# Kernel optimization log

Hardware: AMD Instinct MI355X
Metric: run time of the kernel (lower is better)

The kernel has to match this reference:

```python
import jax, jax.numpy as jnp
import numpy as np

H = 512        # hidden_size
E = 512        # embedding_size
VOCAB = 32
OPS = 16
B = 64         # batch of trees
N = 1023       # complete binary tree, depth 9 (2^10 - 1 nodes)
TEMP = 3.0
INT_TYPES_MAX = 1  # types 0 (INT_PO) and 1 (INT_NE) carry a numeric arg


def setup_inputs() -> dict:
    key = jax.random.key(0)
    ks = jax.random.split(key, 12)
    s = 0.05
    return {
        "node_types": jax.random.randint(ks[0], (B, N), 0, VOCAB),
        "node_args": jax.random.normal(ks[1], (B, N), jnp.float32),
        "validity_mask": jax.random.uniform(ks[2], (B, OPS), jnp.float32, 1e-3, 1.0),
        "emb_table": jax.random.normal(ks[3], (VOCAB, E), jnp.float32) * s,
        "W_ih": jax.random.normal(ks[4], (8 * H, E), jnp.float32) * s,
        "W_hh": jax.random.normal(ks[5], (8 * H, 2 * H), jnp.float32) * s,
        "b_ih": jax.random.normal(ks[6], (8 * H,), jnp.float32) * s,
        "b_hh": jax.random.normal(ks[7], (8 * H,), jnp.float32) * s,
        "W1": jax.random.normal(ks[8], (H, H), jnp.float32) * s,
        "b1": jax.random.normal(ks[9], (H,), jnp.float32) * s,
        "W2": jax.random.normal(ks[10], (OPS, H), jnp.float32) * s,
        "b2": jax.random.normal(ks[11], (OPS,), jnp.float32) * s,
    }


def reference(node_types, node_args, validity_mask, emb_table,
              W_ih, W_hh, b_ih, b_hh, W1, b1, W2, b2):
    # --- SympleEmbedding: per-node embedding; int-typed nodes carry arg in last slot
    emb = emb_table[node_types]                                   # [B, N, E]
    is_int = node_types <= INT_TYPES_MAX                          # [B, N]
    emb = emb.at[..., -1].set(jnp.where(is_int, node_args, emb[..., -1]))

    # --- BinaryTreeLSTM, batched level-by-level (heap layout: children of i are 2i+1, 2i+2)
    D = int(np.log2(N + 1)) - 1                                   # depth of internal levels-1 = 9
    h = jnp.zeros((B, N, H), emb.dtype)                           # leaves: zeros
    c = jnp.zeros((B, N, H), emb.dtype)
    bias = b_ih + b_hh
    for d in range(D - 1, -1, -1):                                # bottom-up over internal levels
        idx = np.arange(2 ** d - 1, 2 ** (d + 1) - 1)             # nodes at level d
        left, right = 2 * idx + 1, 2 * idx + 2
        h0 = jnp.concatenate([h[:, left], h[:, right]], axis=-1)  # [B, n, 2H]
        c0 = jnp.concatenate([c[:, left], c[:, right]], axis=-1)
        gates = (jnp.einsum('bne,ge->bng', emb[:, idx], W_ih)
                 + jnp.einsum('bnh,gh->bng', h0, W_hh) + bias)    # [B, n, 8H]
        i_g, f_g, g_g, o_g = jnp.split(gates, 4, axis=-1)         # torch LSTM gate order i,f,g,o
        c_new = jax.nn.sigmoid(f_g) * c0 + jax.nn.sigmoid(i_g) * jnp.tanh(g_g)
        h_new = jax.nn.sigmoid(o_g) * jnp.tanh(c_new)
        h = h.at[:, idx].set(h_new[..., :H])                      # keep first H (as in module)
        c = c.at[:, idx].set(c_new[..., :H])

    # --- actor FFN on root hidden + validity-masked tempered softmax
    root_h = h[:, 0]                                              # [B, H]
    x = jax.nn.relu(root_h @ W1.T + b1)
    logits = x @ W2.T + b2 + jnp.log(validity_mask)
    return jax.nn.softmax(logits / TEMP, axis=-1)                 # [B, OPS]
```

## Files before the change

kernel.cpp:

```cpp
#include <hip/hip_runtime.h>
#include <hip/hip_cooperative_groups.h>
#include <math.h>

namespace cg = cooperative_groups;

#define Nn 1023

typedef __attribute__((ext_vector_type(8))) short short8;
typedef __attribute__((ext_vector_type(4))) float f32x4;

#define AS1(p) ((const __attribute__((address_space(1))) void*)(p))
#define AS3(p) ((__attribute__((address_space(3))) void*)(p))

__device__ __forceinline__ float sigf(float x) { return 1.0f / (1.0f + __expf(-x)); }
__device__ __forceinline__ float tanhfast(float x) {
    float e = __expf(2.0f * x);
    return 1.0f - 2.0f / (e + 1.0f);
}
__device__ __forceinline__ unsigned short f2bf(float x) {
    unsigned u = __float_as_uint(x);
    return (unsigned short)((u + 0x7fffu + ((u >> 16) & 1u)) >> 16);
}
__device__ __forceinline__ float bf2f(unsigned short b) {
    return __uint_as_float(((unsigned)b) << 16);
}

__global__ __launch_bounds__(256) void prep_all(
    const float* __restrict__ W_hh, unsigned short* __restrict__ WhT,
    const float* __restrict__ W1, float* __restrict__ W1t,
    const int* __restrict__ node_types, const float* __restrict__ node_args,
    const float* __restrict__ emb, const float* __restrict__ W2,
    float* __restrict__ W2t, int* __restrict__ tyv, float* __restrict__ alphaf,
    const float* __restrict__ W_ih, const float* __restrict__ b_ih,
    const float* __restrict__ b_hh, float* __restrict__ E32b,
    float* __restrict__ w511f, int* __restrict__ rowidx, int* __restrict__ cnt) {
    int bid = blockIdx.x, t = threadIdx.x;
    if (bid < 1024) {
        int idx = bid * 256 + t;
        int P = idx >> 7;
        int k0 = (idx & 127) * 8;
        int row = ((P >> 4) & 3) * 1024 + (P >> 6) * 16 + (P & 15);
        const float* src = W_hh + (size_t)row * 1024 + k0;
        float4 v0 = *(const float4*)src;
        float4 v1 = *(const float4*)(src + 4);
        short8 o;
        o[0] = (short)f2bf(v0.x); o[1] = (short)f2bf(v0.y);
        o[2] = (short)f2bf(v0.z); o[3] = (short)f2bf(v0.w);
        o[4] = (short)f2bf(v1.x); o[5] = (short)f2bf(v1.y);
        o[6] = (short)f2bf(v1.z); o[7] = (short)f2bf(v1.w);
        *(short8*)(WhT + (size_t)P * 1024 + k0) = o;
    } else if (bid < 1088) {
        __shared__ float tile[64][65];
        int idx2 = bid - 1024;
        int jb = (idx2 & 7) * 64, kb = (idx2 >> 3) * 64;
        #pragma unroll
        for (int i = 0; i < 16; ++i) {
            int idx = t + i * 256;
            int lj = idx >> 6, lk = idx & 63;
            tile[lj][lk] = W1[(jb + lj) * 512 + kb + lk];
        }
        __syncthreads();
        #pragma unroll
        for (int i = 0; i < 16; ++i) {
            int idx = t + i * 256;
            int lk = idx >> 6, lj = idx & 63;
            W1t[(kb + lk) * 512 + jb + lj] = tile[lj][lk];
        }
    } else if (bid < 1216) {
        int gid = (bid - 1088) * 256 + t;
        if (gid < 32704) {
            int node = gid >> 6, b = gid & 63;
            int ty = node_types[b * Nn + node];
            tyv[gid] = ty;
            alphaf[gid] = (ty <= 1) ? (node_args[b * Nn + node] - emb[ty * 512 + 511]) : 0.f;
        }
        if (gid < 8192) {
            int k = gid >> 4, op = gid & 15;
            W2t[gid] = W2[op * 512 + k];
        }
    } else if (bid < 1472) {
        int o = (bid - 1216) * 256 + t;
        int ty = o >> 11, P = o & 2047;
        int row = ((P >> 4) & 3) * 1024 + (P >> 6) * 16 + (P & 15);
        const float* er = emb + (size_t)ty * 512;
        const float* wr = W_ih + (size_t)row * 512;
        float s0 = b_ih[row] + b_hh[row], s1 = 0.f, s2 = 0.f, s3 = 0.f;
        for (int k = 0; k < 512; k += 16) {
            float4 e0 = *(const float4*)(er + k);
            float4 w0 = *(const float4*)(wr + k);
            float4 e1 = *(const float4*)(er + k + 4);
            float4 w1 = *(const float4*)(wr + k + 4);
            float4 e2 = *(const float4*)(er + k + 8);
            float4 w2 = *(const float4*)(wr + k + 8);
            float4 e3 = *(const float4*)(er + k + 12);
            float4 w3 = *(const float4*)(wr + k + 12);
            s0 = fmaf(e0.x, w0.x, fmaf(e0.y, w0.y, fmaf(e0.z, w0.z, fmaf(e0.w, w0.w, s0))));
            s1 = fmaf(e1.x, w1.x, fmaf(e1.y, w1.y, fmaf(e1.z, w1.z, fmaf(e1.w, w1.w, s1))));
            s2 = fmaf(e2.x, w2.x, fmaf(e2.y, w2.y, fmaf(e2.z, w2.z, fmaf(e2.w, w2.w, s2))));
            s3 = fmaf(e3.x, w3.x, fmaf(e3.y, w3.y, fmaf(e3.z, w3.z, fmaf(e3.w, w3.w, s3))));
        }
        E32b[o] = (s0 + s1) + (s2 + s3);
        if (ty == 0) w511f[P] = wr[511];
    } else {
        int z = (bid - 1472) * 256 + t;
        if (z < 8448) rowidx[z] = 0;
        if (bid == 1472 && t == 0) *cnt = 0;
    }
}

__global__ void zero_out(float* __restrict__ outp, int n) {
    int i = blockIdx.x * 256 + threadIdx.x;
    if (i < n) outp[i] = 0.f;
}

__device__ __forceinline__ void ph0_body(
    int bid,
    const float* __restrict__ E32b, const float* __restrict__ w511f,
    const int* __restrict__ tyv, const float* __restrict__ alphaf,
    unsigned short* __restrict__ Hleaf, float* __restrict__ Cleaf,
    unsigned short* __restrict__ A64,
    unsigned short* __restrict__ Hside, float* __restrict__ Cside,
    int* __restrict__ rowidx, int* __restrict__ cnt) {
    const int t = threadIdx.x;
    if (bid < 64) {
        int o = bid * 256 + t;
        int ty = o >> 9, j = o & 511;
        int Pb = (j >> 4) * 64 + (j & 15);
        const float* Er = E32b + (size_t)ty * 2048;
        float ig = Er[Pb], gg = Er[Pb + 32], og = Er[Pb + 48];
        float cn = sigf(ig) * tanhfast(gg);
        float hn = sigf(og) * tanhfast(cn);
        unsigned short hb = f2bf(hn);
        Hleaf[o] = hb;
        Cleaf[o] = cn;
        A64[ty * 1024 + j] = hb;
        A64[ty * 1024 + 512 + j] = 0;
        A64[(32 + ty) * 1024 + j] = 0;
        A64[(32 + ty) * 1024 + 512 + j] = hb;
    }
    {
        int wave = t >> 6, jc = (t & 63) * 8;
        int r0 = bid * 32 + wave * 8;
        int tys[8];
        #pragma unroll
        for (int i = 0; i < 8; ++i) tys[i] = tyv[16320 + r0 + i];
        #pragma unroll
        for (int i = 0; i < 8; ++i) {
            if (tys[i] > 1) continue;
            int r = r0 + i;
            int gn = 16320 + r;
            float al = alphaf[gn];
            int l = r >> 6, b = r & 63;
            const float* Er = E32b + (size_t)tys[i] * 2048;
            short8 hv;
            float cv[8];
            #pragma unroll
            for (int jj = 0; jj < 8; ++jj) {
                int j = jc + jj;
                int Pb = (j >> 4) * 64 + (j & 15);
                float ig = Er[Pb]      + al * w511f[Pb];
                float gg = Er[Pb + 32] + al * w511f[Pb + 32];
                float og = Er[Pb + 48] + al * w511f[Pb + 48];
                float cn = sigf(ig) * tanhfast(gg);
                float hn = sigf(og) * tanhfast(cn);
                hv[jj] = (short)f2bf(hn);
                cv[jj] = cn;
            }
            *(short8*)(Hside + (size_t)r * 512 + jc) = hv;
            if ((l & 1) == 0) {
                size_t cr = ((size_t)((l >> 1) * 64 + b)) * 512 + jc;
                float4 c0 = {cv[0], cv[1], cv[2], cv[3]};
                float4 c1 = {cv[4], cv[5], cv[6], cv[7]};
                *(float4*)(Cside + cr) = c0;
                *(float4*)(Cside + cr + 4) = c1;
            }
        }
    }
    if (bid >= 64 && bid < 96) {
        int r = (bid - 64) * 256 + t;
        int lf = (r >> 6) * 128 + (r & 63);
        if (tyv[16320 + lf] <= 1 || tyv[16320 + lf + 64] <= 1) {
            int p = atomicAdd(cnt, 1);
            rowidx[p] = r;
        }
    }
}

template<int KT, bool BIAS>
__device__ __forceinline__ void table_gemm_body(
    char* smemraw, const unsigned short* __restrict__ Abf,
    const unsigned short* __restrict__ Bt, const float* __restrict__ biasP,
    float* __restrict__ C0, float* __restrict__ C1, int by) {
    unsigned short* AB = (unsigned short*)smemraw;
    const int t = threadIdx.x;
    const int w = t >> 6, lane = t & 63;
    const int wr = w >> 1, wc = w & 1;
    const int lane15 = lane & 15, lg = lane >> 4;
    const int bcol0 = by * 128;
    const int lanek8 = (lane & 7) * 8;
    const int ROWS = BIAS ? 32 : 64;

    const unsigned short* aA[4];
    const unsigned short* wB[4];
    #pragma unroll
    for (int q = 0; q < 4; ++q) {
        int m = w * 32 + q * 8 + (lane >> 3);
        int r = (m < ROWS) ? m : (ROWS - 1);
        aA[q] = Abf + (size_t)r * (KT * 64);
        int P = bcol0 + w * 32 + q * 8 + (lane >> 3);
        wB[q] = Bt + (size_t)P * (KT * 64);
    }
    auto stage = [&](int kt, int cur) {
        unsigned short* Ad = AB + cur * 16384;
        unsigned short* Bd = Ad + 8192;
        #pragma unroll
        for (int q = 0; q < 4; ++q) {
            __builtin_amdgcn_global_load_lds(AS1(aA[q] + kt * 64 + lanek8),
                                             AS3(Ad + w * 2048 + q * 512), 16, 0, 0);
            __builtin_amdgcn_global_load_lds(AS1(wB[q] + kt * 64 + lanek8),
                                             AS3(Bd + w * 2048 + q * 512), 16, 0, 0);
        }
    };
    stage(0, 0);
    f32x4 acc[4][4];
    int P4[4];
    #pragma unroll
    for (int q = 0; q < 4; ++q) P4[q] = bcol0 + wc * 64 + q * 16 + lane15;
    #pragma unroll
    for (int mi = 0; mi < 4; ++mi)
        #pragma unroll
        for (int reg = 0; reg < 4; ++reg)
            #pragma unroll
            for (int q = 0; q < 4; ++q)
                acc[mi][q][reg] = BIAS ? biasP[P4[q]] : 0.f;
    int cur = 0;
    for (int kt = 0; kt < KT; ++kt) {
        __syncthreads();
        if (kt < KT - 1) stage(kt + 1, cur ^ 1);
        const unsigned short* Ac = AB + cur * 16384;
        const unsigned short* Bc = Ac + 8192;
        #pragma unroll
        for (int ks = 0; ks < 2; ++ks) {
            short8 av[4], bv[4];
            #pragma unroll
            for (int mi = 0; mi < 4; ++mi)
                av[mi] = *(const short8*)(Ac + (wr * 64 + mi * 16 + lane15) * 64 + ks * 32 + lg * 8);
            #pragma unroll
            for (int q = 0; q < 4; ++q)
                bv[q] = *(const short8*)(Bc + (wc * 64 + q * 16 + lane15) * 64 + ks * 32 + lg * 8);
            #pragma unroll
            for (int mi = 0; mi < 4; ++mi)
                #pragma unroll
                for (int q = 0; q < 4; ++q)
                    acc[mi][q] = __builtin_amdgcn_mfma_f32_16x16x32_bf16(av[mi], bv[q], acc[mi][q], 0, 0, 0);
        }
        cur ^= 1;
    }
    #pragma unroll
    for (int mi = 0; mi < 4; ++mi)
        #pragma unroll
        for (int reg = 0; reg < 4; ++reg) {
            int ro = wr * 64 + mi * 16 + lg * 4 + reg;
            #pragma unroll
            for (int q = 0; q < 4; ++q) {
                float v = acc[mi][q][reg];
                if (ro < 32) C0[(size_t)ro * 2048 + P4[q]] = v;
                else if (!BIAS && ro < 64) C1[(size_t)(ro - 32) * 2048 + P4[q]] = v;
            }
        }
    __syncthreads();
}

__device__ __forceinline__ void d7_table_body(
    char* smemraw,
    const float* __restrict__ E32b, const float* __restrict__ GLt,
    const float* __restrict__ GRt, const float* __restrict__ Cleaf,
    const float* __restrict__ w511f,
    const int* __restrict__ tyv, const float* __restrict__ alphaf,
    unsigned short* __restrict__ out_h, float* __restrict__ out_c,
    int bx, int by) {
    float* Es  = (float*)smemraw;
    float* GLs = Es + 32 * 129;
    float* GRs = GLs + 32 * 129;
    float* Cls = GRs + 32 * 129;
    float* w5s = Cls + 32 * 33;
    const int t = threadIdx.x;
    const int j0 = by * 32;
    const int r = bx * 256 + t;

    for (int i = t; i < 32 * 128; i += 256) {
        int ty = i >> 7, pp = i & 127;
        int gp = ((j0 >> 4) + (pp >> 6)) * 64 + (pp & 63);
        Es[ty * 129 + pp]  = E32b[ty * 2048 + gp];
        GLs[ty * 129 + pp] = GLt[ty * 2048 + gp];
        GRs[ty * 129 + pp] = GRt[ty * 2048 + gp];
    }
    for (int i = t; i < 32 * 32; i += 256) {
        int ty = i >> 5, jl = i & 31;
        Cls[ty * 33 + jl] = Cleaf[ty * 512 + j0 + jl];
    }
    if (t < 128) w5s[t] = w511f[((j0 >> 4) + (t >> 6)) * 64 + (t & 63)];
    __syncthreads();

    int gn = 8128 + r;
    int tyP = tyv[gn];
    float aP = alphaf[gn];
    int lf = (r >> 6) * 128 + (r & 63);
    int tyL = tyv[16320 + lf];
    int tyR = tyv[16320 + lf + 64];
    bool skip = (tyL <= 1) || (tyR <= 1);
    bool evenl = (((r >> 6) & 1) == 0);
    size_t crow = ((size_t)((r >> 7) * 64 + (r & 63))) * 512;

    if (!skip) {
        #pragma unroll
        for (int j8 = 0; j8 < 4; ++j8) {
            short8 hv;
            float cv[8];
            #pragma unroll
            for (int jj = 0; jj < 8; ++jj) {
                int jl = j8 * 8 + jj;
                int ppb = (jl >> 4) * 64 + (jl & 15);
                float ig = Es[tyP * 129 + ppb]      + aP * w5s[ppb]      + GLs[tyL * 129 + ppb]      + GRs[tyR * 129 + ppb];
// ... 122 lines not shown
    for (int kt = 0; kt < 16; ++kt) {
        __syncthreads();
        if (kt < 15) stage(kt + 1, cur ^ 1);
        const unsigned short* Ac = AB + cur * 16384;
        const unsigned short* Bc = Ac + 8192;
        #pragma unroll
        for (int ks = 0; ks < 2; ++ks) {
            short8 av[4], bv[4];
            #pragma unroll
            for (int mi = 0; mi < 4; ++mi)
                av[mi] = *(const short8*)(Ac + (wr * 64 + mi * 16 + lane15) * 64 + ks * 32 + lg * 8);
            #pragma unroll
            for (int q = 0; q < 4; ++q)
                bv[q] = *(const short8*)(Bc + (wc * 64 + q * 16 + lane15) * 64 + ks * 32 + lg * 8);
            #pragma unroll
            for (int mi = 0; mi < 4; ++mi)
                #pragma unroll
                for (int q = 0; q < 4; ++q)
                    acc[mi][q] = __builtin_amdgcn_mfma_f32_16x16x32_bf16(av[mi], bv[q], acc[mi][q], 0, 0, 0);
        }
        cur ^= 1;
    }

    const int j = (by * 2 + wc) * 16 + lane15;
    #pragma unroll
    for (int mi = 0; mi < 4; ++mi) {
        #pragma unroll
        for (int reg = 0; reg < 4; ++reg) {
            int r = rr[mi][reg];
            if (r < M) {
                float ig = acc[mi][0][reg];
                float fg = acc[mi][1][reg];
                float gg = acc[mi][2][reg];
                float og = acc[mi][3][reg];
                float cl;
                if (MODE == 2) {
                    int lf = (r >> 6) * 128 + (r & 63);
                    int tyL = tyv[16320 + lf];
                    cl = (tyL <= 1) ? Cside[(size_t)r * 512 + j]
                                    : Cleaf[(size_t)tyL * 512 + j];
                } else {
                    cl = in_c[(size_t)r * 512 + j];
                }
                float cn = sigf(fg) * cl + sigf(ig) * tanhfast(gg);
                float hn = sigf(og) * tanhfast(cn);
                out_h[(size_t)r * 512 + j] = f2bf(hn);
                if (((r >> 6) & 1) == 0)
                    out_c[((size_t)((r >> 7) * 64 + (r & 63))) * 512 + j] = cn;
            }
        }
    }
}

__device__ __forceinline__ void head_body(
    char* smemraw,
    const unsigned short* __restrict__ rootH, const float* __restrict__ W1t,
    const float* __restrict__ b1, const float* __restrict__ W2t,
    const float* __restrict__ b2, const float* __restrict__ vmask,
    float* __restrict__ outp, int b) {
    float* rh = (float*)smemraw;
    float* xs = rh + 512;
    float* part = xs + 512;
    int t = threadIdx.x;
    rh[t] = bf2f(rootH[b * 512 + t]);
    rh[t + 256] = bf2f(rootH[b * 512 + t + 256]);
    __syncthreads();
    #pragma unroll
    for (int jj = 0; jj < 2; ++jj) {
        int jx = t + jj * 256;
        float acc = b1[jx];
        for (int k = 0; k < 512; ++k) acc = fmaf(rh[k], W1t[k * 512 + jx], acc);
        xs[jx] = fmaxf(acc, 0.f);
    }
    __syncthreads();
    int op = t & 15, seg = t >> 4;
    float p = 0.f;
    for (int k = seg * 32; k < seg * 32 + 32; ++k) p = fmaf(xs[k], W2t[k * 16 + op], p);
    part[seg * 17 + op] = p;
    __syncthreads();
    if (t < 16) {
        float s = 0.f;
        #pragma unroll
        for (int g = 0; g < 16; ++g) s += part[g * 17 + t];
        float logit = s + b2[t] + logf(vmask[b * 16 + t]);
        float z = logit * (1.0f / 3.0f);
        float m = z;
        for (int o2 = 8; o2; o2 >>= 1) m = fmaxf(m, __shfl_xor(m, o2, 16));
        float e = __expf(z - m);
        float ssum = e;
        for (int o2 = 8; o2; o2 >>= 1) ssum += __shfl_xor(ssum, o2, 16);
        outp[b * 16 + t] = e / ssum;
    }
}

__global__ __launch_bounds__(256) void tree_main(
    const unsigned short* WhT, const float* E32b, const float* w511f,
    const int* tyv, const float* alphaf,
    unsigned short* Hleaf, unsigned short* Hside,
    float* Cleaf, float* Cside, unsigned short* A64,
    float* GLt, float* GRt, int* rowidx, int* cnt,
    unsigned short* Xh, float* Xc, unsigned short* Yh, float* Yc,
    const float* W1t, const float* b1, const float* W2t, const float* b2,
    const float* vmask, float* outp) {
    cg::grid_group grid = cg::this_grid();
    extern __shared__ char smem[];
    const int bid = blockIdx.x;

    ph0_body(bid, E32b, w511f, tyv, alphaf, Hleaf, Cleaf, A64, Hside, Cside,
             rowidx, cnt);
    __threadfence(); grid.sync();

    if (bid < 16)
        table_gemm_body<16, false>(smem, A64, WhT, nullptr, GLt, GRt, bid);
    __threadfence(); grid.sync();

    d7_table_body(smem, E32b, GLt, GRt, Cleaf, w511f, tyv, alphaf,
                  Xh, Xc, bid & 31, bid >> 5);
    {
        int nc = *cnt;
        int rb = ((nc + 127) & ~127) >> 7;
        for (int T = bid; T < rb * 16; T += 512)
            mfma_tile<2>(smem, WhT, E32b, w511f, tyv, alphaf, nullptr, nullptr,
                         Hleaf, Hside, Cleaf, Cside, rowidx, nc,
                         Xh, Xc, 127, 128, T % rb, T / rb);
    }
    __threadfence(); grid.sync();

    for (int d = 6; d >= 0; --d) {
        int nloc = 1 << d;
        int gx = (nloc >= 2) ? (nloc >> 1) : 1;
        unsigned short* oh = (d & 1) ? Xh : Yh;
        float* oc          = (d & 1) ? Xc : Yc;
        const unsigned short* ih = (d & 1) ? Yh : Xh;
        const float* ic          = (d & 1) ? Yc : Xc;
        int ntiles = gx * 16;
        if (bid < ntiles)
            mfma_tile<0>(smem, WhT, E32b, w511f, tyv, alphaf, ih, ic,
                         nullptr, nullptr, nullptr, nullptr, nullptr, 0,
                         oh, oc, nloc - 1, nloc, bid % gx, bid / gx);
        __threadfence(); grid.sync();
    }

    if (bid < 64)
        head_body(smem, Yh, W1t, b1, W2t, b2, vmask, outp, bid);
}

__global__ __launch_bounds__(256) void ph0_k(
    const float* __restrict__ E32b, const float* __restrict__ w511f,
    const int* __restrict__ tyv, const float* __restrict__ alphaf,
    unsigned short* __restrict__ Hleaf, float* __restrict__ Cleaf,
    unsigned short* __restrict__ A64,
    unsigned short* __restrict__ Hside, float* __restrict__ Cside,
    int* __restrict__ rowidx, int* __restrict__ cnt) {
    ph0_body(blockIdx.x, E32b, w511f, tyv, alphaf, Hleaf, Cleaf, A64,
             Hside, Cside, rowidx, cnt);
}

__global__ __launch_bounds__(256) void glgr_k(
    const unsigned short* __restrict__ A64, const unsigned short* __restrict__ WhT,
    float* __restrict__ GLt, float* __restrict__ GRt) {
    extern __shared__ char smem[];
    table_gemm_body<16, false>(smem, A64, WhT, nullptr, GLt, GRt, blockIdx.x);
}

__global__ __launch_bounds__(256) void d7t_k(
    const float* __restrict__ E32b, const float* __restrict__ GLt,
    const float* __restrict__ GRt, const float* __restrict__ Cleaf,
    const float* __restrict__ w511f,
    const int* __restrict__ tyv, const float* __restrict__ alphaf,
    unsigned short* __restrict__ out_h, float* __restrict__ out_c) {
    extern __shared__ char smem[];
    d7_table_body(smem, E32b, GLt, GRt, Cleaf, w511f, tyv, alphaf,
                  out_h, out_c, blockIdx.x, blockIdx.y);
}

__global__ __launch_bounds__(256) void d7c_k(
    const unsigned short* __restrict__ WhT, const float* __restrict__ E32b,
    const float* __restrict__ w511f,
    const int* __restrict__ tyv, const float* __restrict__ alphaf,
    const unsigned short* __restrict__ Hleaf, const unsigned short* __restrict__ Hside,
    const float* __restrict__ Cleaf, const float* __restrict__ Cside,
    const int* __restrict__ rowidx, const int* __restrict__ cnt,
    unsigned short* __restrict__ out_h, float* __restrict__ out_c) {
    extern __shared__ char smem[];
    int nc = *cnt;
    int padded = (nc + 127) & ~127;
    if ((int)blockIdx.x * 128 >= padded) return;
    mfma_tile<2>(smem, WhT, E32b, w511f, tyv, alphaf, nullptr, nullptr,
                 Hleaf, Hside, Cleaf, Cside, rowidx, nc,
                 out_h, out_c, 127, 128, blockIdx.x, blockIdx.y);
}

__global__ __launch_bounds__(256) void lvl_k(
    const unsigned short* __restrict__ WhT, const float* __restrict__ E32b,
    const float* __restrict__ w511f,
    const int* __restrict__ tyv, const float* __restrict__ alphaf,
    const unsigned short* __restrict__ in_h, const float* __restrict__ in_c,
    unsigned short* __restrict__ out_h, float* __restrict__ out_c,
    int base, int nloc) {
    extern __shared__ char smem[];
    mfma_tile<0>(smem, WhT, E32b, w511f, tyv, alphaf, in_h, in_c,
                 nullptr, nullptr, nullptr, nullptr, nullptr, 0,
                 out_h, out_c, base, nloc, blockIdx.x, blockIdx.y);
}

__global__ __launch_bounds__(256) void head_k(
    const unsigned short* __restrict__ rootH, const float* __restrict__ W1t,
    const float* __restrict__ b1, const float* __restrict__ W2t,
    const float* __restrict__ b2, const float* __restrict__ vmask,
    float* __restrict__ outp) {
    extern __shared__ char smem[];
    head_body(smem, rootH, W1t, b1, W2t, b2, vmask, outp, blockIdx.x);
}

extern "C" void kernel_launch(void* const* d_in, const int* in_sizes, int n_in,
                              void* d_out, int out_size, void* d_ws, size_t ws_size,
                              hipStream_t stream) {
    const int*   node_types = (const int*)d_in[0];
    const float* node_args  = (const float*)d_in[1];
    const float* vmask      = (const float*)d_in[2];
    const float* emb_table  = (const float*)d_in[3];
    const float* W_ih       = (const float*)d_in[4];
    const float* W_hh       = (const float*)d_in[5];
    const float* b_ih       = (const float*)d_in[6];
    const float* b_hh       = (const float*)d_in[7];
    const float* W1         = (const float*)d_in[8];
    const float* b1         = (const float*)d_in[9];
    const float* W2         = (const float*)d_in[10];
    const float* b2         = (const float*)d_in[11];
    float* out = (float*)d_out;

    char* ws = (char*)d_ws;
    size_t off = 0;
    auto alloc = [&](size_t bytes) { char* p = ws + off; off += (bytes + 255) & ~(size_t)255; return p; };
    unsigned short* WhT  = (unsigned short*)alloc((size_t)2048 * 1024 * 2);
    float* E32b          = (float*)alloc((size_t)32 * 2048 * 4);
    float* w511f         = (float*)alloc(2048 * 4);
    float* W1t           = (float*)alloc((size_t)512 * 512 * 4);
    float* W2t           = (float*)alloc(8192 * 4);
    int*   tyv           = (int*)alloc(32704 * 4);
    float* alphaf        = (float*)alloc(32704 * 4);
    unsigned short* Hleaf= (unsigned short*)alloc((size_t)32 * 512 * 2);
    float* Cleaf         = (float*)alloc((size_t)32 * 512 * 4);
    unsigned short* A64  = (unsigned short*)alloc((size_t)64 * 1024 * 2);
    float* GLt           = (float*)alloc((size_t)32 * 2048 * 4);
    float* GRt           = (float*)alloc((size_t)32 * 2048 * 4);
    int*   rowidx        = (int*)alloc(8448 * 4);
    int*   cnt           = (int*)alloc(256);
    unsigned short* Hside= (unsigned short*)alloc((size_t)16384 * 512 * 2);
    float* Cside         = (float*)alloc((size_t)8192 * 512 * 4);
    unsigned short* Xh   = (unsigned short*)alloc((size_t)8192 * 512 * 2);
    unsigned short* Yh   = (unsigned short*)alloc((size_t)4096 * 512 * 2);
    float* Xc            = (float*)alloc((size_t)4096 * 512 * 4);
    float* Yc            = (float*)alloc((size_t)2048 * 512 * 4);

    if (ws_size < off) {
        zero_out<<<(out_size + 255) / 256, 256, 0, stream>>>(out, out_size);
        return;
    }

    prep_all<<<1505, 256, 0, stream>>>(W_hh, WhT, W1, W1t, node_types, node_args,
                                       emb_table, W2, W2t, tyv, alphaf,
                                       W_ih, b_ih, b_hh, E32b, w511f, rowidx, cnt);

    bool coop_ok = false;
    {
        int occ = 0;
        hipError_t qe = hipOccupancyMaxActiveBlocksPerMultiprocessor(
            &occ, tree_main, 256, 65536);
        if (qe == hipSuccess && occ >= 2) coop_ok = true;
    }
    if (coop_ok) {
        const unsigned short* cWhT = WhT;  const float* cE32b = E32b;
        const float* cw511 = w511f;        const int* ctyv = tyv;
        const float* calpha = alphaf;      const float* cW1t = W1t;
        const float* cW2t = W2t;
        void* kargs[] = {
            (void*)&cWhT, (void*)&cE32b, (void*)&cw511, (void*)&ctyv, (void*)&calpha,
            (void*)&Hleaf, (void*)&Hside, (void*)&Cleaf, (void*)&Cside, (void*)&A64,
            (void*)&GLt, (void*)&GRt, (void*)&rowidx, (void*)&cnt,
            (void*)&Xh, (void*)&Xc, (void*)&Yh, (void*)&Yc,
            (void*)&cW1t, (void*)&b1, (void*)&cW2t, (void*)&b2,
            (void*)&vmask, (void*)&out };
        hipError_t le = hipLaunchCooperativeKernel(
            tree_main, dim3(512), dim3(256), kargs, (unsigned)65536, stream);
        if (le != hipSuccess) coop_ok = false;
    }
    if (!coop_ok) {
        ph0_k<<<512, 256, 0, stream>>>(E32b, w511f, tyv, alphaf, Hleaf, Cleaf,
                                       A64, Hside, Cside, rowidx, cnt);
        glgr_k<<<16, 256, 65536, stream>>>(A64, WhT, GLt, GRt);
        d7t_k<<<dim3(32, 16), 256, 54272, stream>>>(
            E32b, GLt, GRt, Cleaf, w511f, tyv, alphaf, Xh, Xc);
        d7c_k<<<dim3(64, 16), 256, 65536, stream>>>(
            WhT, E32b, w511f, tyv, alphaf, Hleaf, Hside, Cleaf, Cside,
            rowidx, cnt, Xh, Xc);
        for (int d = 6; d >= 0; --d) {
            int nloc = 1 << d;
            unsigned short* oh = (d & 1) ? Xh : Yh;
            float* oc          = (d & 1) ? Xc : Yc;
            const unsigned short* ih = (d & 1) ? Yh : Xh;
            const float* ic          = (d & 1) ? Yc : Xc;
            int gx = (nloc >= 2) ? (nloc / 2) : 1;
            lvl_k<<<dim3(gx, 16), 256, 65536, stream>>>(
                WhT, E32b, w511f, tyv, alphaf, ih, ic, oh, oc, nloc - 1, nloc);
        }
        head_k<<<64, 256, 5184, stream>>>(Yh, W1t, b1, W2t, b2, vmask, out);
    }
}
```

Baseline: 384.7 us.

## Replace cooperative launch with custom grid barrier and split-K level GEMMs

Drops the cooperative-groups launch and its multi-kernel fallback in favour of a single 256-block persistent kernel synchronised by a hand-written atomic grid barrier. The per-type embedding gate table moves from a scalar FP32 dot product in prep into an in-kernel bf16 MFMA table GEMM using a pre-converted W_ih. Upper tree levels use split-K MFMA partial products written to a scratch buffer, followed by a separate cell-update pass, so small levels can occupy more blocks. This adds extra barriers and partial-sum traffic, and relies on all 256 blocks being co-resident without a cooperative launch guarantee.

Result: slower. 1.131 ms (+194.0%).

```diff
diff --git a/kernel.cpp b/kernel.cpp
--- a/kernel.cpp
+++ b/kernel.cpp
@@ -1,10 +1,8 @@
 #include <hip/hip_runtime.h>
-#include <hip/hip_cooperative_groups.h>
 #include <math.h>
 
-namespace cg = cooperative_groups;
-
 #define Nn 1023
+#define NB 256
 
 typedef __attribute__((ext_vector_type(8))) short short8;
 typedef __attribute__((ext_vector_type(4))) float f32x4;
@@ -25,15 +23,29 @@
     return __uint_as_float(((unsigned)b) << 16);
 }
 
+__device__ __forceinline__ void gridbar(int* bc, int target) {
+    __syncthreads();
+    if (threadIdx.x == 0) {
+        __threadfence();
+        __hip_atomic_fetch_add(bc, 1, __ATOMIC_ACQ_REL, __HIP_MEMORY_SCOPE_AGENT);
+        while (__hip_atomic_load(bc, __ATOMIC_ACQUIRE, __HIP_MEMORY_SCOPE_AGENT) < target)
+            __builtin_amdgcn_s_sleep(1);
+        __threadfence();
+    }
+    __syncthreads();
+}
+
 __global__ __launch_bounds__(256) void prep_all(
     const float* __restrict__ W_hh, unsigned short* __restrict__ WhT,
+    const float* __restrict__ W_ih, unsigned short* __restrict__ W_iT,
+    float* __restrict__ w511f,
     const float* __restrict__ W1, float* __restrict__ W1t,
     const int* __restrict__ node_types, const float* __restrict__ node_args,
     const float* __restrict__ emb, const float* __restrict__ W2,
     float* __restrict__ W2t, int* __restrict__ tyv, float* __restrict__ alphaf,
-    const float* __restrict__ W_ih, const float* __restrict__ b_ih,
-    const float* __restrict__ b_hh, float* __restrict__ E32b,
-    float* __restrict__ w511f, int* __restrict__ rowidx, int* __restrict__ cnt) {
+    const float* __restrict__ b_ih, const float* __restrict__ b_hh,
+    float* __restrict__ biasP, unsigned short* __restrict__ A64e,
+    int* __restrict__ rowidx, int* __restrict__ cnt) {
     int bid = blockIdx.x, t = threadIdx.x;
     if (bid < 1024) {
         int idx = bid * 256 + t;
@@ -49,9 +61,24 @@
         o[4] = (short)f2bf(v1.x); o[5] = (short)f2bf(v1.y);
         o[6] = (short)f2bf(v1.z); o[7] = (short)f2bf(v1.w);
         *(short8*)(WhT + (size_t)P * 1024 + k0) = o;
-    } else if (bid < 1088) {
+    } else if (bid < 1536) {
+        int idx = (bid - 1024) * 256 + t;
+        int P = idx >> 6;
+        int k0 = (idx & 63) * 8;
+        int row = ((P >> 4) & 3) * 1024 + (P >> 6) * 16 + (P & 15);
+        const float* src = W_ih + (size_t)row * 512 + k0;
+        float4 v0 = *(const float4*)src;
+        float4 v1 = *(const float4*)(src + 4);
+        short8 o;
+        o[0] = (short)f2bf(v0.x); o[1] = (short)f2bf(v0.y);
+        o[2] = (short)f2bf(v0.z); o[3] = (short)f2bf(v0.w);
+        o[4] = (short)f2bf(v1.x); o[5] = (short)f2bf(v1.y);
+        o[6] = (short)f2bf(v1.z); o[7] = (short)f2bf(v1.w);
+        *(short8*)(W_iT + (size_t)P * 512 + k0) = o;
+        if (k0 == 504) w511f[P] = v1.w;
+    } else if (bid < 1600) {
         __shared__ float tile[64][65];
-        int idx2 = bid - 1024;
+        int idx2 = bid - 1536;
         int jb = (idx2 & 7) * 64, kb = (idx2 >> 3) * 64;
         #pragma unroll
         for (int i = 0; i < 16; ++i) {
@@ -66,8 +93,8 @@
             int lk = idx >> 6, lj = idx & 63;
             W1t[(kb + lk) * 512 + jb + lj] = tile[lj][lk];
         }
-    } else if (bid < 1216) {
-        int gid = (bid - 1088) * 256 + t;
+    } else if (bid < 1728) {
+        int gid = (bid - 1600) * 256 + t;
         if (gid < 32704) {
             int node = gid >> 6, b = gid & 63;
             int ty = node_types[b * Nn + node];
@@ -78,39 +105,104 @@
             int k = gid >> 4, op = gid & 15;
             W2t[gid] = W2[op * 512 + k];
         }
-    } else if (bid < 1472) {
-        int o = (bid - 1216) * 256 + t;
-        int ty = o >> 11, P = o & 2047;
-        int row = ((P >> 4) & 3) * 1024 + (P >> 6) * 16 + (P & 15);
-        const float* er = emb + (size_t)ty * 512;
-        const float* wr = W_ih + (size_t)row * 512;
-        float s0 = b_ih[row] + b_hh[row], s1 = 0.f, s2 = 0.f, s3 = 0.f;
-        for (int k = 0; k < 512; k += 16) {
-            float4 e0 = *(const float4*)(er + k);
-            float4 w0 = *(const float4*)(wr + k);
-            float4 e1 = *(const float4*)(er + k + 4);
-            float4 w1 = *(const float4*)(wr + k + 4);
-            float4 e2 = *(const float4*)(er + k + 8);
-            float4 w2 = *(const float4*)(wr + k + 8);
-            float4 e3 = *(const float4*)(er + k + 12);
-            float4 w3 = *(const float4*)(wr + k + 12);
-            s0 = fmaf(e0.x, w0.x, fmaf(e0.y, w0.y, fmaf(e0.z, w0.z, fmaf(e0.w, w0.w, s0))));
-            s1 = fmaf(e1.x, w1.x, fmaf(e1.y, w1.y, fmaf(e1.z, w1.z, fmaf(e1.w, w1.w, s1))));
-            s2 = fmaf(e2.x, w2.x, fmaf(e2.y, w2.y, fmaf(e2.z, w2.z, fmaf(e2.w, w2.w, s2))));
-            s3 = fmaf(e3.x, w3.x, fmaf(e3.y, w3.y, fmaf(e3.z, w3.z, fmaf(e3.w, w3.w, s3))));
-        }
-        E32b[o] = (s0 + s1) + (s2 + s3);
-        if (ty == 0) w511f[P] = wr[511];
+        if (gid < 2048) {
+            int row = ((gid >> 4) & 3) * 1024 + (gid >> 6) * 16 + (gid & 15);
+            biasP[gid] = b_ih[row] + b_hh[row];
+        }
+    } else if (bid < 1792) {
+        int o = (bid - 1728) * 256 + t;
+        A64e[o] = f2bf(emb[o]);
     } else {
-        int z = (bid - 1472) * 256 + t;
+        int z = (bid - 1792) * 256 + t;
         if (z < 8448) rowidx[z] = 0;
-        if (bid == 1472 && t == 0) *cnt = 0;
+        if (bid == 1792 && t < 64) cnt[t] = 0;
     }
 }
 
 __global__ void zero_out(float* __restrict__ outp, int n) {
     int i = blockIdx.x * 256 + threadIdx.x;
     if (i < n) outp[i] = 0.f;
+}
+
+template<int KT, int NROW>
+__device__ __forceinline__ void table_gemm_body(
+    char* smemraw, const unsigned short* __restrict__ Abf,
+    const unsigned short* __restrict__ Bt, const float* __restrict__ biasP,
+    float* __restrict__ C0, float* __restrict__ C1, int by) {
+    unsigned short* AB = (unsigned short*)smemraw;
+    const int t = threadIdx.x;
+    const int w = t >> 6, lane = t & 63;
+    const int wr = w >> 1, wc = w & 1;
+    const int lane15 = lane & 15, lg = lane >> 4;
+    const int bcol0 = by * 128;
+    const int lanek8 = (lane & 7) * 8;
+
+    const unsigned short* aA[4];
+    const unsigned short* wB[4];
+    #pragma unroll
+    for (int q = 0; q < 4; ++q) {
+        int m = w * 32 + q * 8 + (lane >> 3);
+        int r = (m < NROW) ? m : (NROW - 1);
+        aA[q] = Abf + (size_t)r * (KT * 64);
+        int P = bcol0 + w * 32 + q * 8 + (lane >> 3);
+        wB[q] = Bt + (size_t)P * (KT * 64);
+    }
+    auto stage = [&](int kt, int cur) {
+        unsigned short* Ad = AB + cur * 16384;
+        unsigned short* Bd = Ad + 8192;
+        #pragma unroll
+        for (int q = 0; q < 4; ++q) {
+            __builtin_amdgcn_global_load_lds(AS1(aA[q] + kt * 64 + lanek8),
+                                             AS3(Ad + w * 2048 + q * 512), 16, 0, 0);
+            __builtin_amdgcn_global_load_lds(AS1(wB[q] + kt * 64 + lanek8),
+                                             AS3(Bd + w * 2048 + q * 512), 16, 0, 0);
+        }
+    };
+    stage(0, 0);
+    f32x4 acc[4][4] = {};
+    int P4[4];
+    #pragma unroll
+    for (int q = 0; q < 4; ++q) P4[q] = bcol0 + wc * 64 + q * 16 + lane15;
+    int cur = 0;
+    for (int kt = 0; kt < KT; ++kt) {
+        __syncthreads();
+        if (kt < KT - 1) stage(kt + 1, cur ^ 1);
+        const unsigned short* Ac = AB + cur * 16384;
+        const unsigned short* Bc = Ac + 8192;
+        #pragma unroll
+        for (int ks = 0; ks < 2; ++ks) {
+            short8 av[4], bv[4];
+            #pragma unroll
+            for (int mi = 0; mi < 4; ++mi)
+                av[mi] = *(const short8*)(Ac + (wr * 64 + mi * 16 + lane15) * 64 + ks * 32 + lg * 8);
+            #pragma unroll
+            for (int q = 0; q < 4; ++q)
+                bv[q] = *(const short8*)(Bc + (wc * 64 + q * 16 + lane15) * 64 + ks * 32 + lg * 8);
+            #pragma unroll
+            for (int mi = 0; mi < 4; ++mi)
+                #pragma unroll
+                for (int q = 0; q < 4; ++q)
+                    acc[mi][q] = __builtin_amdgcn_mfma_f32_16x16x32_bf16(av[mi], bv[q], acc[mi][q], 0, 0, 0);
+        }
+        cur ^= 1;
+    }
+    #pragma unroll
+    for (int mi = 0; mi < 4; ++mi)
+        #pragma unroll
+        for (int reg = 0; reg < 4; ++reg) {
+            int ro = wr * 64 + mi * 16 + lg * 4 + reg;
+            #pragma unroll
+            for (int q = 0; q < 4; ++q) {
+                float v = acc[mi][q][reg];
+                if (NROW == 32) {
+                    if (ro < 32) C0[(size_t)ro * 2048 + P4[q]] = v + biasP[P4[q]];
+                } else {
+                    if (ro < 32) C0[(size_t)ro * 2048 + P4[q]] = v;
+                    else if (ro < 64) C1[(size_t)(ro - 32) * 2048 + P4[q]] = v;
+                }
+            }
+        }
+    __syncthreads();
 }
 
 __device__ __forceinline__ void ph0_body(
@@ -140,18 +232,16 @@
     }
     {
         int wave = t >> 6, jc = (t & 63) * 8;
-        int r0 = bid * 32 + wave * 8;
-        int tys[8];
-        #pragma unroll
-        for (int i = 0; i < 8; ++i) tys[i] = tyv[16320 + r0 + i];
-        #pragma unroll
-        for (int i = 0; i < 8; ++i) {
-            if (tys[i] > 1) continue;
+        int r0 = bid * 64 + wave * 16;
+        #pragma unroll
+        for (int i = 0; i < 16; ++i) {
             int r = r0 + i;
             int gn = 16320 + r;
+            int ty = tyv[gn];
+            if (ty > 1) continue;
             float al = alphaf[gn];
             int l = r >> 6, b = r & 63;
-            const float* Er = E32b + (size_t)tys[i] * 2048;
+            const float* Er = E32b + (size_t)ty * 2048;
             short8 hv;
             float cv[8];
             #pragma unroll
@@ -184,91 +274,6 @@
             rowidx[p] = r;
         }
     }
-}
-
-template<int KT, bool BIAS>
-__device__ __forceinline__ void table_gemm_body(
-    char* smemraw, const unsigned short* __restrict__ Abf,
-    const unsigned short* __restrict__ Bt, const float* __restrict__ biasP,
-    float* __restrict__ C0, float* __restrict__ C1, int by) {
-    unsigned short* AB = (unsigned short*)smemraw;
-    const int t = threadIdx.x;
-    const int w = t >> 6, lane = t & 63;
-    const int wr = w >> 1, wc = w & 1;
-    const int lane15 = lane & 15, lg = lane >> 4;
-    const int bcol0 = by * 128;
-    const int lanek8 = (lane & 7) * 8;
-    const int ROWS = BIAS ? 32 : 64;
-
-    const unsigned short* aA[4];
-    const unsigned short* wB[4];
-    #pragma unroll
-    for (int q = 0; q < 4; ++q) {
-        int m = w * 32 + q * 8 + (lane >> 3);
-        int r = (m < ROWS) ? m : (ROWS - 1);
-        aA[q] = Abf + (size_t)r * (KT * 64);
-        int P = bcol0 + w * 32 + q * 8 + (lane >> 3);
-        wB[q] = Bt + (size_t)P * (KT * 64);
-    }
-    auto stage = [&](int kt, int cur) {
-        unsigned short* Ad = AB + cur * 16384;
-        unsigned short* Bd = Ad + 8192;
-        #pragma unroll
-        for (int q = 0; q < 4; ++q) {
-            __builtin_amdgcn_global_load_lds(AS1(aA[q] + kt * 64 + lanek8),
-                                             AS3(Ad + w * 2048 + q * 512), 16, 0, 0);
-            __builtin_amdgcn_global_load_lds(AS1(wB[q] + kt * 64 + lanek8),
-                                             AS3(Bd + w * 2048 + q * 512), 16, 0, 0);
-        }
-    };
-    stage(0, 0);
-    f32x4 acc[4][4];
-    int P4[4];
-    #pragma unroll
-    for (int q = 0; q < 4; ++q) P4[q] = bcol0 + wc * 64 + q * 16 + lane15;
-    #pragma unroll
-    for (int mi = 0; mi < 4; ++mi)
-        #pragma unroll
-        for (int reg = 0; reg < 4; ++reg)
-            #pragma unroll
-            for (int q = 0; q < 4; ++q)
-                acc[mi][q][reg] = BIAS ? biasP[P4[q]] : 0.f;
-    int cur = 0;
-    for (int kt = 0; kt < KT; ++kt) {
-        __syncthreads();
-        if (kt < KT - 1) stage(kt + 1, cur ^ 1);
-        const unsigned short* Ac = AB + cur * 16384;
-        const unsigned short* Bc = Ac + 8192;
-        #pragma unroll
-        for (int ks = 0; ks < 2; ++ks) {
-            short8 av[4], bv[4];
-            #pragma unroll
-            for (int mi = 0; mi < 4; ++mi)
-                av[mi] = *(const short8*)(Ac + (wr * 64 + mi * 16 + lane15) * 64 + ks * 32 + lg * 8);
-            #pragma unroll
-            for (int q = 0; q < 4; ++q)
-                bv[q] = *(const short8*)(Bc + (wc * 64 + q * 16 + lane15) * 64 + ks * 32 + lg * 8);
-            #pragma unroll
-            for (int mi = 0; mi < 4; ++mi)
-                #pragma unroll
-                for (int q = 0; q < 4; ++q)
-                    acc[mi][q] = __builtin_amdgcn_mfma_f32_16x16x32_bf16(av[mi], bv[q], acc[mi][q], 0, 0, 0);
-        }
-        cur ^= 1;
-    }
-    #pragma unroll
-    for (int mi = 0; mi < 4; ++mi)
-        #pragma unroll
-        for (int reg = 0; reg < 4; ++reg) {
-            int ro = wr * 64 + mi * 16 + lg * 4 + reg;
-            #pragma unroll
-            for (int q = 0; q < 4; ++q) {
-                float v = acc[mi][q][reg];
-                if (ro < 32) C0[(size_t)ro * 2048 + P4[q]] = v;
-                else if (!BIAS && ro < 64) C1[(size_t)(ro - 32) * 2048 + P4[q]] = v;
-            }
-        }
-    __syncthreads();
 }
 
 __device__ __forceinline__ void d7_table_body(
@@ -497,6 +502,140 @@
     }
 }
 
+__device__ __forceinline__ void mfma_split_body(
+    char* smemraw, const unsigned short* __restrict__ WhT,
+    const unsigned short* __restrict__ in_h, float* __restrict__ Gp,
+    int Mrows, int kt0, int nkt, int bx, int by) {
+    unsigned short* AB = (unsigned short*)smemraw;
+    const int t = threadIdx.x;
+    const int w = t >> 6, lane = t & 63;
+    const int wr = w >> 1, wc = w & 1;
+    const int lane15 = lane & 15, lg = lane >> 4;
+    const int brow0 = bx * 128;
+    const int bcol0 = by * 128;
+    const int lanek8 = (lane & 7) * 8;
+
+    const unsigned short* baseL[4];
+    const unsigned short* baseR[4];
+    const unsigned short* wB[4];
+    #pragma unroll
+    for (int q = 0; q < 4; ++q) {
+        int m = w * 32 + q * 8 + (lane >> 3);
+        int r = brow0 + m; if (r > Mrows - 1) r = Mrows - 1;
+        int lf = (r >> 6) * 128 + (r & 63);
+        baseL[q] = in_h + (size_t)lf * 512;
+        baseR[q] = baseL[q] + 64 * 512;
+        int P = bcol0 + w * 32 + q * 8 + (lane >> 3);
+        wB[q] = WhT + (size_t)P * 1024;
+    }
+    auto stage = [&](int kt, int cur) {
+        unsigned short* Ad = AB + cur * 16384;
+        unsigned short* Bd = Ad + 8192;
+        #pragma unroll
+        for (int q = 0; q < 4; ++q) {
+            const unsigned short* s = (kt < 8) ? (baseL[q] + kt * 64)
+                                               : (baseR[q] + (kt - 8) * 64);
+            __builtin_amdgcn_global_load_lds(AS1(s + lanek8),
+                                             AS3(Ad + w * 2048 + q * 512), 16, 0, 0);
+            __builtin_amdgcn_global_load_lds(AS1(wB[q] + kt * 64 + lanek8),
+                                             AS3(Bd + w * 2048 + q * 512), 16, 0, 0);
+        }
+    };
+    stage(kt0, 0);
+    f32x4 acc[4][4] = {};
+    int P4[4];
+    int rr[4][4];
+    #pragma unroll
+    for (int q = 0; q < 4; ++q) P4[q] = bcol0 + wc * 64 + q * 16 + lane15;
+    #pragma unroll
+    for (int mi = 0; mi < 4; ++mi)
+        #pragma unroll
+        for (int reg = 0; reg < 4; ++reg) {
+            int r = brow0 + wr * 64 + mi * 16 + lg * 4 + reg;
+            if (r > Mrows - 1) r = Mrows - 1;
+            rr[mi][reg] = r;
+        }
+    int cur = 0;
+    for (int i = 0; i < nkt; ++i) {
+        __syncthreads();
+        if (i < nkt - 1) stage(kt0 + i + 1, cur ^ 1);
+        const unsigned short* Ac = AB + cur * 16384;
+        const unsigned short* Bc = Ac + 8192;
+        #pragma unroll
+        for (int ks = 0; ks < 2; ++ks) {
+            short8 av[4], bv[4];
+            #pragma unroll
+            for (int mi = 0; mi < 4; ++mi)
+                av[mi] = *(const short8*)(Ac + (wr * 64 + mi * 16 + lane15) * 64 + ks * 32 + lg * 8);
+            #pragma unroll
+            for (int q = 0; q < 4; ++q)
+                bv[q] = *(const short8*)(Bc + (wc * 64 + q * 16 + lane15) * 64 + ks * 32 + lg * 8);
+            #pragma unroll
+            for (int mi = 0; mi < 4; ++mi)
+                #pragma unroll
+                for (int q = 0; q < 4; ++q)
+                    acc[mi][q] = __builtin_amdgcn_mfma_f32_16x16x32_bf16(av[mi], bv[q], acc[mi][q], 0, 0, 0);
+        }
+        cur ^= 1;
+    }
+    #pragma unroll
+    for (int mi = 0; mi < 4; ++mi)
+        #pragma unroll
+        for (int reg = 0; reg < 4; ++reg) {
+            int r = rr[mi][reg];
+            #pragma unroll
+            for (int q = 0; q < 4; ++q)
+                Gp[(size_t)r * 2048 + P4[q]] = acc[mi][q][reg];
+        }
+    __syncthreads();
+}
+
+__device__ __forceinline__ void cell_split_body(
+    int bid, const float* __restrict__ Gpart, int KS, int Mrows, int base,
+    const float* __restrict__ E32b, const float* __restrict__ w511f,
+    const int* __restrict__ tyv, const float* __restrict__ alphaf,
+    const float* __restrict__ in_c,
+    unsigned short* __restrict__ out_h, float* __restrict__ out_c) {
+    int total = Mrows * 64;
+    for (int idx = bid * 256 + threadIdx.x; idx < total; idx += NB * 256) {
+        int r = idx >> 6;
+        int jc = (idx & 63) * 8;
+        int gn = base * 64 + r;
+        int ty = tyv[gn];
+        float al = alphaf[gn];
+        const float* Er = E32b + (size_t)ty * 2048;
+        short8 hv;
+        float cv[8];
+        #pragma unroll
+        for (int jj = 0; jj < 8; ++jj) {
+            int j = jc + jj;
+            int Pb = (j >> 4) * 64 + (j & 15);
+            float g[4];
+            #pragma unroll
+            for (int q = 0; q < 4; ++q) {
+                int P = Pb + q * 16;
+                float s = Er[P] + al * w511f[P];
+                for (int ks = 0; ks < KS; ++ks)
+                    s += Gpart[((size_t)ks * Mrows + r) * 2048 + P];
+                g[q] = s;
+            }
+            float cl = in_c[(size_t)r * 512 + j];
+            float cn = sigf(g[1]) * cl + sigf(g[0]) * tanhfast(g[2]);
+            float hn = sigf(g[3]) * tanhfast(cn);
+            hv[jj] = (short)f2bf(hn);
+            cv[jj] = cn;
+        }
+        *(short8*)(out_h + (size_t)r * 512 + jc) = hv;
+        if (((r >> 6) & 1) == 0) {
+            size_t cr = ((size_t)((r >> 7) * 64 + (r & 63))) * 512 + jc;
+            float4 c0 = {cv[0], cv[1], cv[2], cv[3]};
+            float4 c1 = {cv[4], cv[5], cv[6], cv[7]};
+            *(float4*)(out_c + cr) = c0;
+            *(float4*)(out_c + cr + 4) = c1;
+        }
+    }
+}
+
 __device__ __forceinline__ void head_body(
     char* smemraw,
     const unsigned short* __restrict__ rootH, const float* __restrict__ W1t,
@@ -539,123 +678,93 @@
 }
 
 __global__ __launch_bounds__(256) void tree_main(
-    const unsigned short* WhT, const float* E32b, const float* w511f,
+    const unsigned short* WhT, const unsigned short* W_iT,
+    const unsigned short* A64e, const float* biasP,
+    float* E32b, const float* w511f,
     const int* tyv, const float* alphaf,
     unsigned short* Hleaf, unsigned short* Hside,
     float* Cleaf, float* Cside, unsigned short* A64,
-    float* GLt, float* GRt, int* rowidx, int* cnt,
+    float* GLt, float* GRt, int* rowidx, int* cnt, float* Gpart,
     unsigned short* Xh, float* Xc, unsigned short* Yh, float* Yc,
     const float* W1t, const float* b1, const float* W2t, const float* b2,
     const float* vmask, float* outp) {
-    cg::grid_group grid = cg::this_grid();
     extern __shared__ char smem[];
     const int bid = blockIdx.x;
+    int* bc = cnt + 32;
+    int bt = 0;
+
+    if (bid < 16)
+        table_gemm_body<8, 32>(smem, A64e, W_iT, biasP, E32b, nullptr, bid);
+    bt += NB; gridbar(bc, bt);
 
     ph0_body(bid, E32b, w511f, tyv, alphaf, Hleaf, Cleaf, A64, Hside, Cside,
              rowidx, cnt);
-    __threadfence(); grid.sync();
+    bt += NB; gridbar(bc, bt);
 
     if (bid < 16)
-        table_gemm_body<16, false>(smem, A64, WhT, nullptr, GLt, GRt, bid);
-    __threadfence(); grid.sync();
-
-    d7_table_body(smem, E32b, GLt, GRt, Cleaf, w511f, tyv, alphaf,
-                  Xh, Xc, bid & 31, bid >> 5);
+        table_gemm_body<16, 64>(smem, A64, WhT, nullptr, GLt, GRt, bid);
+    bt += NB; gridbar(bc, bt);
+
+    for (int T = bid; T < 512; T += NB)
+        d7_table_body(smem, E32b, GLt, GRt, Cleaf, w511f, tyv, alphaf,
+                      Xh, Xc, T & 31, T >> 5);
     {
-        int nc = *cnt;
+        int nc = __hip_atomic_load(cnt, __ATOMIC_ACQUIRE, __HIP_MEMORY_SCOPE_AGENT);
         int rb = ((nc + 127) & ~127) >> 7;
-        for (int T = bid; T < rb * 16; T += 512)
+        for (int T = bid; T < rb * 16; T += NB)
             mfma_tile<2>(smem, WhT, E32b, w511f, tyv, alphaf, nullptr, nullptr,
                          Hleaf, Hside, Cleaf, Cside, rowidx, nc,
                          Xh, Xc, 127, 128, T % rb, T / rb);
     }
-    __threadfence(); grid.sync();
-
-    for (int d = 6; d >= 0; --d) {
+    bt += NB; gridbar(bc, bt);
+
+    for (int d = 6; d >= 3; --d) {
         int nloc = 1 << d;
-        int gx = (nloc >= 2) ? (nloc >> 1) : 1;
+        int gx = nloc >> 1;
         unsigned short* oh = (d & 1) ? Xh : Yh;
         float* oc          = (d & 1) ? Xc : Yc;
         const unsigned short* ih = (d & 1) ? Yh : Xh;
         const float* ic          = (d & 1) ? Yc : Xc;
         int ntiles = gx * 16;
-        if (bid < ntiles)
+        for (int T = bid; T < ntiles; T += NB)
             mfma_tile<0>(smem, WhT, E32b, w511f, tyv, alphaf, ih, ic,
                          nullptr, nullptr, nullptr, nullptr, nullptr, 0,
-                         oh, oc, nloc - 1, nloc, bid % gx, bid / gx);
-        __threadfence(); grid.sync();
+                         oh, oc, nloc - 1, nloc, T % gx, T / gx);
+        bt += NB; gridbar(bc, bt);
+    }
+
+    {
+        const int dv[3]  = {2, 1, 0};
+        const int KSv[3] = {4, 8, 8};
+        const int kpv[3] = {4, 2, 2};
+        const int rtv[3] = {2, 1, 1};
+        #pragma unroll
+        for (int s = 0; s < 3; ++s) {
+            int d = dv[s];
+            int nloc = 1 << d;
+            int M = nloc * 64;
+            int KS = KSv[s], ktpb = kpv[s], rt = rtv[s];
+            unsigned short* oh = (d & 1) ? Xh : Yh;
+            float* oc          = (d & 1) ? Xc : Yc;
+            const unsigned short* ih = (d & 1) ? Yh : Xh;
+            const float* ic          = (d & 1) ? Yc : Xc;
+            int nblk = rt * 16 * KS;
+            if (bid < nblk) {
+                int bx = bid % rt;
+                int by = (bid / rt) % 16;
+                int ks = bid / (rt * 16);
+                mfma_split_body(smem, WhT, ih, Gpart + (size_t)ks * M * 2048,
+                                M, ks * ktpb, ktpb, bx, by);
+            }
+            bt += NB; gridbar(bc, bt);
+            cell_split_body(bid, Gpart, KS, M, nloc - 1, E32b, w511f, tyv,
+                            alphaf, ic, oh, oc);
+            bt += NB; gridbar(bc, bt);
+        }
     }
 
     if (bid < 64)
         head_body(smem, Yh, W1t, b1, W2t, b2, vmask, outp, bid);
-}
-
-__global__ __launch_bounds__(256) void ph0_k(
-    const float* __restrict__ E32b, const float* __restrict__ w511f,
-    const int* __restrict__ tyv, const float* __restrict__ alphaf,
-    unsigned short* __restrict__ Hleaf, float* __restrict__ Cleaf,
-    unsigned short* __restrict__ A64,
-    unsigned short* __restrict__ Hside, float* __restrict__ Cside,
-    int* __restrict__ rowidx, int* __restrict__ cnt) {
-    ph0_body(blockIdx.x, E32b, w511f, tyv, alphaf, Hleaf, Cleaf, A64,
-             Hside, Cside, rowidx, cnt);
-}
-
-__global__ __launch_bounds__(256) void glgr_k(
-    const unsigned short* __restrict__ A64, const unsigned short* __restrict__ WhT,
-    float* __restrict__ GLt, float* __restrict__ GRt) {
-    extern __shared__ char smem[];
-    table_gemm_body<16, false>(smem, A64, WhT, nullptr, GLt, GRt, blockIdx.x);
-}
-
-__global__ __launch_bounds__(256) void d7t_k(
-    const float* __restrict__ E32b, const float* __restrict__ GLt,
-    const float* __restrict__ GRt, const float* __restrict__ Cleaf,
-    const float* __restrict__ w511f,
-    const int* __restrict__ tyv, const float* __restrict__ alphaf,
-    unsigned short* __restrict__ out_h, float* __restrict__ out_c) {
-    extern __shared__ char smem[];
-    d7_table_body(smem, E32b, GLt, GRt, Cleaf, w511f, tyv, alphaf,
-                  out_h, out_c, blockIdx.x, blockIdx.y);
-}
-
-__global__ __launch_bounds__(256) void d7c_k(
-    const unsigned short* __restrict__ WhT, const float* __restrict__ E32b,
-    const float* __restrict__ w511f,
-    const int* __restrict__ tyv, const float* __restrict__ alphaf,
-    const unsigned short* __restrict__ Hleaf, const unsigned short* __restrict__ Hside,
-    const float* __restrict__ Cleaf, const float* __restrict__ Cside,
-    const int* __restrict__ rowidx, const int* __restrict__ cnt,
-    unsigned short* __restrict__ out_h, float* __restrict__ out_c) {
-    extern __shared__ char smem[];
-    int nc = *cnt;
-    int padded = (nc + 127) & ~127;
-    if ((int)blockIdx.x * 128 >= padded) return;
-    mfma_tile<2>(smem, WhT, E32b, w511f, tyv, alphaf, nullptr, nullptr,
-                 Hleaf, Hside, Cleaf, Cside, rowidx, nc,
-                 out_h, out_c, 127, 128, blockIdx.x, blockIdx.y);
-}
-
-__global__ __launch_bounds__(256) void lvl_k(
-    const unsigned short* __restrict__ WhT, const float* __restrict__ E32b,
-    const float* __restrict__ w511f,
-    const int* __restrict__ tyv, const float* __restrict__ alphaf,
-    const unsigned short* __restrict__ in_h, const float* __restrict__ in_c,
-    unsigned short* __restrict__ out_h, float* __restrict__ out_c,
-    int base, int nloc) {
-    extern __shared__ char smem[];
-    mfma_tile<0>(smem, WhT, E32b, w511f, tyv, alphaf, in_h, in_c,
-                 nullptr, nullptr, nullptr, nullptr, nullptr, 0,
-                 out_h, out_c, base, nloc, blockIdx.x, blockIdx.y);
-}
-
-__global__ __launch_bounds__(256) void head_k(
-    const unsigned short* __restrict__ rootH, const float* __restrict__ W1t,
-    const float* __restrict__ b1, const float* __restrict__ W2t,
-    const float* __restrict__ b2, const float* __restrict__ vmask,
-    float* __restrict__ outp) {
-    extern __shared__ char smem[];
-    head_body(smem, rootH, W1t, b1, W2t, b2, vmask, outp, blockIdx.x);
 }
 
 extern "C" void kernel_launch(void* const* d_in, const int* in_sizes, int n_in,
@@ -679,8 +788,10 @@
     size_t off = 0;
     auto alloc = [&](size_t bytes) { char* p = ws + off; off += (bytes + 255) & ~(size_t)255; return p; };
     unsigned short* WhT  = (unsigned short*)alloc((size_t)2048 * 1024 * 2);
+    unsigned short* W_iT = (unsigned short*)alloc((size_t)2048 * 512 * 2);
     float* E32b          = (float*)alloc((size_t)32 * 2048 * 4);
     float* w511f         = (float*)alloc(2048 * 4);
+    float* biasP         = (float*)alloc(2048 * 4);
     float* W1t           = (float*)alloc((size_t)512 * 512 * 4);
     float* W2t           = (float*)alloc(8192 * 4);
     int*   tyv           = (int*)alloc(32704 * 4);
@@ -688,10 +799,12 @@
     unsigned short* Hleaf= (unsigned short*)alloc((size_t)32 * 512 * 2);
     float* Cleaf         = (float*)alloc((size_t)32 * 512 * 4);
     unsigned short* A64  = (unsigned short*)alloc((size_t)64 * 1024 * 2);
+    unsigned short* A64e = (unsigned short*)alloc((size_t)32 * 512 * 2);
     float* GLt           = (float*)alloc((size_t)32 * 2048 * 4);
     float* GRt           = (float*)alloc((size_t)32 * 2048 * 4);
     int*   rowidx        = (int*)alloc(8448 * 4);
     int*   cnt           = (int*)alloc(256);
+    float* Gpart         = (float*)alloc((size_t)8 * 256 * 2048 * 4);
     unsigned short* Hside= (unsigned short*)alloc((size_t)16384 * 512 * 2);
     float* Cside         = (float*)alloc((size_t)8192 * 512 * 4);
     unsigned short* Xh   = (unsigned short*)alloc((size_t)8192 * 512 * 2);
@@ -704,52 +817,12 @@
         return;
     }
 
-    prep_all<<<1505, 256, 0, stream>>>(W_hh, WhT, W1, W1t, node_types, node_args,
-                                       emb_table, W2, W2t, tyv, alphaf,
-                                       W_ih, b_ih, b_hh, E32b, w511f, rowidx, cnt);
-
-    bool coop_ok = false;
-    {
-        int occ = 0;
-        hipError_t qe = hipOccupancyMaxActiveBlocksPerMultiprocessor(
-            &occ, tree_main, 256, 65536);
-        if (qe == hipSuccess && occ >= 2) coop_ok = true;
-    }
-    if (coop_ok) {
-        const unsigned short* cWhT = WhT;  const float* cE32b = E32b;
-        const float* cw511 = w511f;        const int* ctyv = tyv;
-        const float* calpha = alphaf;      const float* cW1t = W1t;
-        const float* cW2t = W2t;
-        void* kargs[] = {
-            (void*)&cWhT, (void*)&cE32b, (void*)&cw511, (void*)&ctyv, (void*)&calpha,
-            (void*)&Hleaf, (void*)&Hside, (void*)&Cleaf, (void*)&Cside, (void*)&A64,
-            (void*)&GLt, (void*)&GRt, (void*)&rowidx, (void*)&cnt,
-            (void*)&Xh, (void*)&Xc, (void*)&Yh, (void*)&Yc,
-            (void*)&cW1t, (void*)&b1, (void*)&cW2t, (void*)&b2,
-            (void*)&vmask, (void*)&out };
-        hipError_t le = hipLaunchCooperativeKernel(
-            tree_main, dim3(512), dim3(256), kargs, (unsigned)65536, stream);
-        if (le != hipSuccess) coop_ok = false;
-    }
-    if (!coop_ok) {
-        ph0_k<<<512, 256, 0, stream>>>(E32b, w511f, tyv, alphaf, Hleaf, Cleaf,
-                                       A64, Hside, Cside, rowidx, cnt);
-        glgr_k<<<16, 256, 65536, stream>>>(A64, WhT, GLt, GRt);
-        d7t_k<<<dim3(32, 16), 256, 54272, stream>>>(
-            E32b, GLt, GRt, Cleaf, w511f, tyv, alphaf, Xh, Xc);
-        d7c_k<<<dim3(64, 16), 256, 65536, stream>>>(
-            WhT, E32b, w511f, tyv, alphaf, Hleaf, Hside, Cleaf, Cside,
-            rowidx, cnt, Xh, Xc);
-        for (int d = 6; d >= 0; --d) {
-            int nloc = 1 << d;
-            unsigned short* oh = (d & 1) ? Xh : Yh;
-            float* oc          = (d & 1) ? Xc : Yc;
-            const unsigned short* ih = (d & 1) ? Yh : Xh;
-            const float* ic          = (d & 1) ? Yc : Xc;
-            int gx = (nloc >= 2) ? (nloc / 2) : 1;
-            lvl_k<<<dim3(gx, 16), 256, 65536, stream>>>(
-                WhT, E32b, w511f, tyv, alphaf, ih, ic, oh, oc, nloc - 1, nloc);
-        }
-        head_k<<<64, 256, 5184, stream>>>(Yh, W1t, b1, W2t, b2, vmask, out);
-    }
-}
+    prep_all<<<1825, 256, 0, stream>>>(
+        W_hh, WhT, W_ih, W_iT, w511f, W1, W1t, node_types, node_args,
+        emb_table, W2, W2t, tyv, alphaf, b_ih, b_hh, biasP, A64e, rowidx, cnt);
+
+    tree_main<<<NB, 256, 65536, stream>>>(
+        WhT, W_iT, A64e, biasP, E32b, w511f, tyv, alphaf,
+        Hleaf, Hside, Cleaf, Cside, A64, GLt, GRt, rowidx, cnt, Gpart,
+        Xh, Xc, Yh, Yc, W1t, b1, W2t, b2, vmask, out);
+}
```
